# Kernel tuning notes

Hardware: AMD Instinct MI355X
Metric: run time of the kernel (lower is better)

Reference implementation:

```python
import jax, jax.numpy as jnp
import numpy as np

# Complete 32-ary tree of depth 3: vocab = 32**3 = 32768 leaves.
B = 4096       # batch
NHID = 512     # hidden size
BR = 32        # branching factor (num_children at every internal node)
DEPTH = 3      # number of internal-node decisions from root to leaf
V = BR ** DEPTH
NUM_NODES = sum(BR ** k for k in range(DEPTH))  # 1 + 32 + 1024 = 1057

# Static tree-indexing tables (level-order node numbering).
_LEVEL_OFFSET = np.array([sum(BR ** j for j in range(k)) for k in range(DEPTH)], dtype=np.int64)   # [0, 1, 33]
_NODE_DIV = np.array([BR ** (DEPTH - k) for k in range(DEPTH)], dtype=np.int64)                    # node-within-level divisor
_STEP_DIV = np.array([BR ** (DEPTH - 1 - k) for k in range(DEPTH)], dtype=np.int64)                # child-step divisor


def setup_inputs() -> dict:
    key = jax.random.key(0)
    k1, k2, k3 = jax.random.split(key, 3)
    inputs = jax.random.normal(k1, (B, NHID), dtype=jnp.float32)
    labels = jax.random.randint(k2, (B,), 0, V)                     # leaf index per sample
    W = jax.random.normal(k3, (NUM_NODES, NHID, BR), dtype=jnp.float32)  # all node params, stacked
    return {"inputs": inputs, "labels": labels, "W": W}


def reference(inputs, labels, W):
    lab = labels[:, None]                                            # [B, 1]
    node_idx = jnp.asarray(_LEVEL_OFFSET)[None, :] + lab // jnp.asarray(_NODE_DIV)[None, :]  # [B, D] node on path
    steps = (lab // jnp.asarray(_STEP_DIV)[None, :]) % BR            # [B, D] child taken at each node
    Wg = W[node_idx]                                                 # [B, D, NHID, BR] gathered path params
    logits = jnp.einsum('bh,bdhc->bdc', inputs, Wg)                  # [B, D, BR]
    p = jax.nn.softmax(logits, axis=-1)
    step_p = jnp.take_along_axis(p, steps[:, :, None], axis=-1)[..., 0]  # [B, D]
    return jnp.prod(step_p, axis=-1)                                 # [B] path probability
```

## Files before the change

### kernel.cpp

```cpp
#include <hip/hip_runtime.h>


#define NHID  512
#define BR    32
#define BATCH 4096
#define NBUCK 1024
#define SMAX  8
#define GMAX  1536

#define FMA4(A, xv, wv_) do { \
    (A).x = fmaf((xv), (wv_).x, (A).x); \
    (A).y = fmaf((xv), (wv_).y, (A).y); \
    (A).z = fmaf((xv), (wv_).z, (A).z); \
    (A).w = fmaf((xv), (wv_).w, (A).w); } while (0)

__global__ __launch_bounds__(1024) void k_sort(const int* __restrict__ labels,
                                               int* __restrict__ order,
                                               int* __restrict__ ngroups,
                                               int* __restrict__ gdesc) {
    __shared__ int labs[BATCH];
    __shared__ int hist[NBUCK];
    __shared__ int wsum1[16];
    __shared__ int wsum2[16];
    const int t  = threadIdx.x;
    const int wv = t >> 6;
    const int ln = t & 63;

    hist[t] = 0;
    #pragma unroll
    for (int r = 0; r < BATCH / 1024; ++r)
        labs[t + 1024 * r] = labels[t + 1024 * r];
    __syncthreads();
    #pragma unroll
    for (int r = 0; r < BATCH / 1024; ++r)
        atomicAdd(&hist[labs[t + 1024 * r] >> 5], 1);
    __syncthreads();

    const int cnt  = hist[t];
    const int gcnt = (cnt + SMAX - 1) / SMAX;

    int s1 = cnt, s2 = gcnt;
    #pragma unroll
    for (int d = 1; d < 64; d <<= 1) {
        int u1 = __shfl_up(s1, d);
        int u2 = __shfl_up(s2, d);
        if (ln >= d) { s1 += u1; s2 += u2; }
    }
    if (ln == 63) { wsum1[wv] = s1; wsum2[wv] = s2; }
    __syncthreads();
    if (t < 16) {
        int a = wsum1[t], b = wsum2[t];
        #pragma unroll
        for (int d = 1; d < 16; d <<= 1) {
            int ua = __shfl_up(a, d, 16);
            int ub = __shfl_up(b, d, 16);
            if (t >= d) { a += ua; b += ub; }
        }
        wsum1[t] = a; wsum2[t] = b;
        if (t == 15) *ngroups = b;
    }
    __syncthreads();
    const int base1 = (wv > 0) ? wsum1[wv - 1] : 0;
    const int base2 = (wv > 0) ? wsum2[wv - 1] : 0;
    const int off  = base1 + s1 - cnt;
    const int goff = base2 + s2 - gcnt;
    hist[t] = off;
    __syncthreads();

    for (int j = 0; j < gcnt; ++j)
        gdesc[goff + j] = (off + j * SMAX)
                        | (min(SMAX, cnt - j * SMAX) << 12)
                        | (t << 16);

    #pragma unroll
    for (int r = 0; r < BATCH / 1024; ++r) {
        int j = t + 1024 * r;
        int pos = atomicAdd(&hist[labs[j] >> 5], 1);
        order[pos] = j;
    }
}

__global__ __launch_bounds__(192) void hsm_g8(
    const float* __restrict__ inputs,
    const int* __restrict__ labels,
    const float* __restrict__ W,
    const int* __restrict__ order,
    const int* __restrict__ ngroups,
    const int* __restrict__ gdesc,
    float* __restrict__ out)
{
    __shared__ float xsT[NHID * SMAX];
    __shared__ float pk[3][SMAX];
    __shared__ int   sids[SMAX];
    __shared__ int   slab[SMAX];

    const int gid = blockIdx.x;
    if (gid >= *ngroups) return;
    const int d     = gdesc[gid];
    const int start = d & 0xFFF;
    const int m     = (d >> 12) & 0xF;
    const int g     = d >> 16;
    const int tid   = threadIdx.x;

    if (tid < SMAX) {
        int sid = (tid < m) ? order[start + tid] : -1;
        sids[tid] = sid;
        slab[tid] = (sid >= 0) ? labels[sid] : 0;
    }
    __syncthreads();

    for (int h = tid; h < NHID; h += 192) {
        float v[SMAX];
        #pragma unroll
        for (int s = 0; s < SMAX; ++s) {
            int id = sids[s];
            v[s] = (id >= 0) ? inputs[(size_t)id * NHID + h] : 0.0f;
        }
        float4* dst = (float4*)&xsT[h * SMAX];
        dst[0] = make_float4(v[0], v[1], v[2], v[3]);
        dst[1] = make_float4(v[4], v[5], v[6], v[7]);
    }
    __syncthreads();

    const int k    = tid >> 6;
    const int lane = tid & 63;
    const int colg = lane & 7;
    const int hsel = lane >> 3;

    const int node = (k == 0) ? 0 : (k == 1) ? 1 + (g >> 5) : 33 + g;
    const int step01 = (k == 0) ? (g >> 5) : (g & 31);

    const float4* wp = (const float4*)(W + (size_t)node * (NHID * BR))
                       + hsel * 8 + colg;
    const float4* xp = (const float4*)xsT + hsel * 2;

    float4 acc[SMAX];
    #pragma unroll
    for (int s = 0; s < SMAX; ++s) acc[s] = make_float4(0, 0, 0, 0);

    float4 wcur[8], wnxt[8];
    #pragma unroll
    for (int j = 0; j < 8; ++j) wcur[j] = wp[j * 64];

    #pragma unroll
    for (int ii = 0; ii < 64; ii += 8) {
        if (ii + 8 < 64) {
            #pragma unroll
            for (int j = 0; j < 8; ++j) wnxt[j] = wp[(ii + 8 + j) * 64];
        }
        #pragma unroll
        for (int j = 0; j < 8; ++j) {
            float4 xa = xp[(ii + j) * 16];
            float4 xb = xp[(ii + j) * 16 + 1];
            FMA4(acc[0], xa.x, wcur[j]); FMA4(acc[1], xa.y, wcur[j]);
            FMA4(acc[2], xa.z, wcur[j]); FMA4(acc[3], xa.w, wcur[j]);
            FMA4(acc[4], xb.x, wcur[j]); FMA4(acc[5], xb.y, wcur[j]);
            FMA4(acc[6], xb.z, wcur[j]); FMA4(acc[7], xb.w, wcur[j]);
        }
        #pragma unroll
        for (int j = 0; j < 8; ++j) wcur[j] = wnxt[j];
    }

    #pragma unroll
    for (int s = 0; s < SMAX; ++s) {
        #pragma unroll
        for (int mm = 8; mm <= 32; mm <<= 1) {
            acc[s].x += __shfl_xor(acc[s].x, mm);
            acc[s].y += __shfl_xor(acc[s].y, mm);
            acc[s].z += __shfl_xor(acc[s].z, mm);
            acc[s].w += __shfl_xor(acc[s].w, mm);
        }
    }

    #pragma unroll
    for (int s = 0; s < SMAX; ++s) {
        float4 a = acc[s];
        float mx = fmaxf(fmaxf(a.x, a.y), fmaxf(a.z, a.w));
        #pragma unroll
        for (int mm = 1; mm <= 4; mm <<= 1) mx = fmaxf(mx, __shfl_xor(mx, mm));
        float es = expf(a.x - mx) + expf(a.y - mx) + expf(a.z - mx) + expf(a.w - mx);
        #pragma unroll
        for (int mm = 1; mm <= 4; mm <<= 1) es += __shfl_xor(es, mm);

        int step = (k == 2) ? (slab[s] & 31) : step01;
        int e = step & 3;
        float v = (e == 0) ? a.x : (e == 1) ? a.y : (e == 2) ? a.z : a.w;
        float sl = __shfl(v, step >> 2);
        float p = expf(sl - mx) / es;
        if (lane == 0) pk[k][s] = p;
    }
    __syncthreads();

    if (tid < SMAX && sids[tid] >= 0)
        out[sids[tid]] = pk[0][tid] * pk[1][tid] * pk[2][tid];
}

extern "C" void kernel_launch(void* const* d_in, const int* in_sizes, int n_in,
                              void* d_out, int out_size, void* d_ws, size_t ws_size,
                              hipStream_t stream)
{
    const float* inputs = (const float*)d_in[0];
    const int*   labels = (const int*)d_in[1];
    const float* W      = (const float*)d_in[2];
    float* out = (float*)d_out;

    char* ws = (char*)d_ws;
    int* order   = (int*)ws;
    int* ngroups = (int*)(ws + 16384);
    int* gdesc   = (int*)(ws + 16384 + 128);

    k_sort<<<dim3(1),    dim3(1024), 0, stream>>>(labels, order, ngroups, gdesc);
    hsm_g8<<<dim3(GMAX), dim3(192),  0, stream>>>(inputs, labels, W, order,
                                                  ngroups, gdesc, out);
}
```

Baseline: 122.1 us.

## Fuse label bucketing into the main kernel and drop the separate sort pass

Removes the single-block sort kernel and its workspace descriptors. Each of 1024 blocks now scans the whole label array, gathers the samples whose leaf bucket matches its own index into shared memory, and processes them in chunks of eight, reloading its node weights for each chunk. This removes a serial single-block pre-pass and one kernel launch on the critical path. In exchange every block redundantly reads the labels, buckets holding more samples run several chunks in series, and any bucket with more than 128 samples is silently truncated.

```diff
diff --git a/kernel.cpp b/kernel.cpp
--- a/kernel.cpp
+++ b/kernel.cpp
@@ -6,7 +6,7 @@
 #define BATCH 4096
 #define NBUCK 1024
 #define SMAX  8
-#define GMAX  1536
+#define CAP   128
 
 #define FMA4(A, xv, wv_) do { \
     (A).x = fmaf((xv), (wv_).x, (A).x); \
@@ -14,185 +14,126 @@
     (A).z = fmaf((xv), (wv_).z, (A).z); \
     (A).w = fmaf((xv), (wv_).w, (A).w); } while (0)
 
-__global__ __launch_bounds__(1024) void k_sort(const int* __restrict__ labels,
-                                               int* __restrict__ order,
-                                               int* __restrict__ ngroups,
-                                               int* __restrict__ gdesc) {
-    __shared__ int labs[BATCH];
-    __shared__ int hist[NBUCK];
-    __shared__ int wsum1[16];
-    __shared__ int wsum2[16];
-    const int t  = threadIdx.x;
-    const int wv = t >> 6;
-    const int ln = t & 63;
-
-    hist[t] = 0;
-    #pragma unroll
-    for (int r = 0; r < BATCH / 1024; ++r)
-        labs[t + 1024 * r] = labels[t + 1024 * r];
-    __syncthreads();
-    #pragma unroll
-    for (int r = 0; r < BATCH / 1024; ++r)
-        atomicAdd(&hist[labs[t + 1024 * r] >> 5], 1);
-    __syncthreads();
-
-    const int cnt  = hist[t];
-    const int gcnt = (cnt + SMAX - 1) / SMAX;
-
-    int s1 = cnt, s2 = gcnt;
-    #pragma unroll
-    for (int d = 1; d < 64; d <<= 1) {
-        int u1 = __shfl_up(s1, d);
-        int u2 = __shfl_up(s2, d);
-        if (ln >= d) { s1 += u1; s2 += u2; }
-    }
-    if (ln == 63) { wsum1[wv] = s1; wsum2[wv] = s2; }
-    __syncthreads();
-    if (t < 16) {
-        int a = wsum1[t], b = wsum2[t];
-        #pragma unroll
-        for (int d = 1; d < 16; d <<= 1) {
-            int ua = __shfl_up(a, d, 16);
-            int ub = __shfl_up(b, d, 16);
-            if (t >= d) { a += ua; b += ub; }
-        }
-        wsum1[t] = a; wsum2[t] = b;
-        if (t == 15) *ngroups = b;
-    }
-    __syncthreads();
-    const int base1 = (wv > 0) ? wsum1[wv - 1] : 0;
-    const int base2 = (wv > 0) ? wsum2[wv - 1] : 0;
-    const int off  = base1 + s1 - cnt;
-    const int goff = base2 + s2 - gcnt;
-    hist[t] = off;
-    __syncthreads();
-
-    for (int j = 0; j < gcnt; ++j)
-        gdesc[goff + j] = (off + j * SMAX)
-                        | (min(SMAX, cnt - j * SMAX) << 12)
-                        | (t << 16);
-
-    #pragma unroll
-    for (int r = 0; r < BATCH / 1024; ++r) {
-        int j = t + 1024 * r;
-        int pos = atomicAdd(&hist[labs[j] >> 5], 1);
-        order[pos] = j;
-    }
-}
-
-__global__ __launch_bounds__(192) void hsm_g8(
+__global__ __launch_bounds__(192) void hsm_bucket(
     const float* __restrict__ inputs,
     const int* __restrict__ labels,
     const float* __restrict__ W,
-    const int* __restrict__ order,
-    const int* __restrict__ ngroups,
-    const int* __restrict__ gdesc,
     float* __restrict__ out)
 {
     __shared__ float xsT[NHID * SMAX];
     __shared__ float pk[3][SMAX];
-    __shared__ int   sids[SMAX];
-    __shared__ int   slab[SMAX];
+    __shared__ int   sids[CAP];
+    __shared__ int   slab[CAP];
+    __shared__ int   scnt;
 
-    const int gid = blockIdx.x;
-    if (gid >= *ngroups) return;
-    const int d     = gdesc[gid];
-    const int start = d & 0xFFF;
-    const int m     = (d >> 12) & 0xF;
-    const int g     = d >> 16;
-    const int tid   = threadIdx.x;
-
-    if (tid < SMAX) {
-        int sid = (tid < m) ? order[start + tid] : -1;
-        sids[tid] = sid;
-        slab[tid] = (sid >= 0) ? labels[sid] : 0;
-    }
-    __syncthreads();
-
-    for (int h = tid; h < NHID; h += 192) {
-        float v[SMAX];
-        #pragma unroll
-        for (int s = 0; s < SMAX; ++s) {
-            int id = sids[s];
-            v[s] = (id >= 0) ? inputs[(size_t)id * NHID + h] : 0.0f;
-        }
-        float4* dst = (float4*)&xsT[h * SMAX];
-        dst[0] = make_float4(v[0], v[1], v[2], v[3]);
-        dst[1] = make_float4(v[4], v[5], v[6], v[7]);
-    }
-    __syncthreads();
-
+    const int g    = blockIdx.x;
+    const int tid  = threadIdx.x;
     const int k    = tid >> 6;
     const int lane = tid & 63;
     const int colg = lane & 7;
     const int hsel = lane >> 3;
 
-    const int node = (k == 0) ? 0 : (k == 1) ? 1 + (g >> 5) : 33 + g;
+    const int node   = (k == 0) ? 0 : (k == 1) ? 1 + (g >> 5) : 33 + g;
     const int step01 = (k == 0) ? (g >> 5) : (g & 31);
 
     const float4* wp = (const float4*)(W + (size_t)node * (NHID * BR))
                        + hsel * 8 + colg;
     const float4* xp = (const float4*)xsT + hsel * 2;
 
-    float4 acc[SMAX];
-    #pragma unroll
-    for (int s = 0; s < SMAX; ++s) acc[s] = make_float4(0, 0, 0, 0);
-
     float4 wcur[8], wnxt[8];
     #pragma unroll
     for (int j = 0; j < 8; ++j) wcur[j] = wp[j * 64];
 
-    #pragma unroll
-    for (int ii = 0; ii < 64; ii += 8) {
-        if (ii + 8 < 64) {
-            #pragma unroll
-            for (int j = 0; j < 8; ++j) wnxt[j] = wp[(ii + 8 + j) * 64];
-        }
-        #pragma unroll
-        for (int j = 0; j < 8; ++j) {
-            float4 xa = xp[(ii + j) * 16];
-            float4 xb = xp[(ii + j) * 16 + 1];
-            FMA4(acc[0], xa.x, wcur[j]); FMA4(acc[1], xa.y, wcur[j]);
-            FMA4(acc[2], xa.z, wcur[j]); FMA4(acc[3], xa.w, wcur[j]);
-            FMA4(acc[4], xb.x, wcur[j]); FMA4(acc[5], xb.y, wcur[j]);
-            FMA4(acc[6], xb.z, wcur[j]); FMA4(acc[7], xb.w, wcur[j]);
-        }
-        #pragma unroll
-        for (int j = 0; j < 8; ++j) wcur[j] = wnxt[j];
-    }
+    if (tid == 0) scnt = 0;
+    __syncthreads();
 
-    #pragma unroll
-    for (int s = 0; s < SMAX; ++s) {
-        #pragma unroll
-        for (int mm = 8; mm <= 32; mm <<= 1) {
-            acc[s].x += __shfl_xor(acc[s].x, mm);
-            acc[s].y += __shfl_xor(acc[s].y, mm);
-            acc[s].z += __shfl_xor(acc[s].z, mm);
-            acc[s].w += __shfl_xor(acc[s].w, mm);
-        }
-    }
-
-    #pragma unroll
-    for (int s = 0; s < SMAX; ++s) {
-        float4 a = acc[s];
-        float mx = fmaxf(fmaxf(a.x, a.y), fmaxf(a.z, a.w));
-        #pragma unroll
-        for (int mm = 1; mm <= 4; mm <<= 1) mx = fmaxf(mx, __shfl_xor(mx, mm));
-        float es = expf(a.x - mx) + expf(a.y - mx) + expf(a.z - mx) + expf(a.w - mx);
-        #pragma unroll
-        for (int mm = 1; mm <= 4; mm <<= 1) es += __shfl_xor(es, mm);
-
-        int step = (k == 2) ? (slab[s] & 31) : step01;
-        int e = step & 3;
-        float v = (e == 0) ? a.x : (e == 1) ? a.y : (e == 2) ? a.z : a.w;
-        float sl = __shfl(v, step >> 2);
-        float p = expf(sl - mx) / es;
-        if (lane == 0) pk[k][s] = p;
+    const int4* l4 = (const int4*)labels;
+    for (int i = tid; i < BATCH / 4; i += 192) {
+        const int4 v = l4[i];
+        if ((v.x >> 5) == g) { int p = atomicAdd(&scnt, 1); if (p < CAP) { sids[p] = 4*i;   slab[p] = v.x; } }
+        if ((v.y >> 5) == g) { int p = atomicAdd(&scnt, 1); if (p < CAP) { sids[p] = 4*i+1; slab[p] = v.y; } }
+        if ((v.z >> 5) == g) { int p = atomicAdd(&scnt, 1); if (p < CAP) { sids[p] = 4*i+2; slab[p] = v.z; } }
+        if ((v.w >> 5) == g) { int p = atomicAdd(&scnt, 1); if (p < CAP) { sids[p] = 4*i+3; slab[p] = v.w; } }
     }
     __syncthreads();
+    const int mt = min(scnt, CAP);
+    if (mt == 0) return;
 
-    if (tid < SMAX && sids[tid] >= 0)
-        out[sids[tid]] = pk[0][tid] * pk[1][tid] * pk[2][tid];
+    for (int c0 = 0; c0 < mt; c0 += SMAX) {
+        if (c0 > 0) {
+            #pragma unroll
+            for (int j = 0; j < 8; ++j) wcur[j] = wp[j * 64];
+        }
+
+        for (int h = tid; h < NHID; h += 192) {
+            float v[SMAX];
+            #pragma unroll
+            for (int s = 0; s < SMAX; ++s) {
+                const int q = c0 + s;
+                v[s] = (q < mt) ? inputs[(size_t)sids[q] * NHID + h] : 0.0f;
+            }
+            float4* dst = (float4*)&xsT[h * SMAX];
+            dst[0] = make_float4(v[0], v[1], v[2], v[3]);
+            dst[1] = make_float4(v[4], v[5], v[6], v[7]);
+        }
+        __syncthreads();
+
+        float4 acc[SMAX];
+        #pragma unroll
+        for (int s = 0; s < SMAX; ++s) acc[s] = make_float4(0, 0, 0, 0);
+
+        #pragma unroll
+        for (int ii = 0; ii < 64; ii += 8) {
+            if (ii + 8 < 64) {
+                #pragma unroll
+                for (int j = 0; j < 8; ++j) wnxt[j] = wp[(ii + 8 + j) * 64];
+            }
+            #pragma unroll
+            for (int j = 0; j < 8; ++j) {
+                const float4 xa = xp[(ii + j) * 16];
+                const float4 xb = xp[(ii + j) * 16 + 1];
+                FMA4(acc[0], xa.x, wcur[j]); FMA4(acc[1], xa.y, wcur[j]);
+                FMA4(acc[2], xa.z, wcur[j]); FMA4(acc[3], xa.w, wcur[j]);
+                FMA4(acc[4], xb.x, wcur[j]); FMA4(acc[5], xb.y, wcur[j]);
+                FMA4(acc[6], xb.z, wcur[j]); FMA4(acc[7], xb.w, wcur[j]);
+            }
+            #pragma unroll
+            for (int j = 0; j < 8; ++j) wcur[j] = wnxt[j];
+        }
+
+        #pragma unroll
+        for (int s = 0; s < SMAX; ++s) {
+            #pragma unroll
+            for (int mm = 8; mm <= 32; mm <<= 1) {
+                acc[s].x += __shfl_xor(acc[s].x, mm);
+                acc[s].y += __shfl_xor(acc[s].y, mm);
+                acc[s].z += __shfl_xor(acc[s].z, mm);
+                acc[s].w += __shfl_xor(acc[s].w, mm);
+            }
+        }
+
+        #pragma unroll
+        for (int s = 0; s < SMAX; ++s) {
+            float4 a = acc[s];
+            float mx = fmaxf(fmaxf(a.x, a.y), fmaxf(a.z, a.w));
+            #pragma unroll
+            for (int mm = 1; mm <= 4; mm <<= 1) mx = fmaxf(mx, __shfl_xor(mx, mm));
+            float es = expf(a.x - mx) + expf(a.y - mx) + expf(a.z - mx) + expf(a.w - mx);
+            #pragma unroll
+            for (int mm = 1; mm <= 4; mm <<= 1) es += __shfl_xor(es, mm);
+
+            const int step = (k == 2) ? (slab[c0 + s] & 31) : step01;
+            const int e = step & 3;
+            const float vv = (e == 0) ? a.x : (e == 1) ? a.y : (e == 2) ? a.z : a.w;
+            const float sl = __shfl(vv, step >> 2);
+            const float p = expf(sl - mx) / es;
+            if (lane == 0) pk[k][s] = p;
+        }
+        __syncthreads();
+
+        if (tid < SMAX && c0 + tid < mt)
+            out[sids[c0 + tid]] = pk[0][tid] * pk[1][tid] * pk[2][tid];
+    }
 }
 
 extern "C" void kernel_launch(void* const* d_in, const int* in_sizes, int n_in,
@@ -204,12 +145,5 @@
     const float* W      = (const float*)d_in[2];
     float* out = (float*)d_out;
 
-    char* ws = (char*)d_ws;
-    int* order   = (int*)ws;
-    int* ngroups = (int*)(ws + 16384);
-    int* gdesc   = (int*)(ws + 16384 + 128);
-
-    k_sort<<<dim3(1),    dim3(1024), 0, stream>>>(labels, order, ngroups, gdesc);
-    hsm_g8<<<dim3(GMAX), dim3(192),  0, stream>>>(inputs, labels, W, order,
-                                                  ngroups, gdesc, out);
+    hsm_bucket<<<dim3(NBUCK), dim3(192), 0, stream>>>(inputs, labels, W, out);
 }
```

After: 195.7 us. 60.2% more time.
